# Kernel optimization log

Hardware: AMD Instinct MI355X
Metric: run time of the kernel (lower is better)

Reference implementation:

```python
import jax, jax.numpy as jnp
from jax import lax
import numpy as np

STEPSZ = 0.1
ALPHA = 0.01
BETA = 0.01
FLTRSTD = 2.0
NSTEPS = 20
DMAX = 15.0
EXTGRADFAC = 10.0
CHUNK = 32  # node chunk size for distance-map render


def _gauss_edge_fltr(std):
    # Gaussian-derivative edge filters, one per spatial axis: [2, 1, K, K]
    r = int(np.ceil(3 * std))
    x = np.arange(-r, r + 1, dtype=np.float32)
    g = np.exp(-x ** 2 / (2 * std ** 2)).astype(np.float32)
    g /= g.sum()
    dg = (-x / std ** 2) * g
    f0 = np.outer(dg, g)   # d/d(axis0)
    f1 = np.outer(g, dg)   # d/d(axis1)
    return np.stack([f0, f1])[:, None].astype(np.float32)


def _snake_matrix(n, alpha, beta, stepsz):
    # implicit internal-energy step matrix (I + t*(alpha*D2 + beta*D2@D2))^-1, open chain
    D = 2 * np.eye(n) - np.eye(n, k=1) - np.eye(n, k=-1)
    D[0, 0] = 1.0
    D[-1, -1] = 1.0
    A = alpha * D + beta * (D @ D)
    return np.linalg.inv(np.eye(n) + stepsz * A).astype(np.float32)


def _bilerp(img, pts):
    # img [H,W], pts [N,2] (row, col) -> [N]
    H, W = img.shape
    r = jnp.clip(pts[:, 0], 0.0, H - 1.0)
    c = jnp.clip(pts[:, 1], 0.0, W - 1.0)
    r0 = jnp.floor(r).astype(jnp.int32)
    c0 = jnp.floor(c).astype(jnp.int32)
    r1 = jnp.minimum(r0 + 1, H - 1)
    c1 = jnp.minimum(c0 + 1, W - 1)
    fr = r - r0
    fc = c - c0
    return (img[r0, c0] * (1 - fr) * (1 - fc) + img[r1, c0] * fr * (1 - fc)
            + img[r0, c1] * (1 - fr) * fc + img[r1, c1] * fr * fc)


def setup_inputs() -> dict:
    key = jax.random.key(0)
    k1, k2, k3 = jax.random.split(key, 3)
    B, H, W, N = 8, 512, 512, 256
    pred_dmap = jax.random.normal(k1, (B, 1, H, W), dtype=jnp.float32)
    node_pos = jax.random.uniform(k2, (B, N, 2), dtype=jnp.float32) * jnp.array([H - 1.0, W - 1.0], dtype=jnp.float32)
    widths = jax.random.uniform(k3, (B, N), dtype=jnp.float32) * 3.0 + 1.0
    return {"pred_dmap": pred_dmap, "node_pos": node_pos, "widths": widths}


def reference(pred_dmap, node_pos, widths):
    B, _, H, W = pred_dmap.shape
    N = node_pos.shape[1]

    # gradient image: conv with Gaussian-derivative filters, scaled (cmptGradIm)
    fltr = jnp.asarray(_gauss_edge_fltr(FLTRSTD))
    gimg = lax.conv_general_dilated(
        pred_dmap, fltr, (1, 1), 'SAME',
        dimension_numbers=('NCHW', 'OIHW', 'NCHW')) * EXTGRADFAC  # [B,2,H,W]

    M = jnp.asarray(_snake_matrix(N, ALPHA, BETA, STEPSZ))  # [N,N]

    def force(g, pts):  # g [2,H,W], pts [N,2] -> [N,2]
        return jnp.stack([_bilerp(g[0], pts), _bilerp(g[1], pts)], axis=-1)

    force_b = jax.vmap(force)
    bounds = jnp.array([H - 1.0, W - 1.0], dtype=pred_dmap.dtype)

    def opt_step(pos, _):
        f = force_b(gimg, pos)                                   # [B,N,2]
        pos = jnp.einsum('nm,bmd->bnd', M, pos + STEPSZ * f)
        pos = jnp.clip(pos, 0.0, bounds)
        return pos, None

    pos, _ = lax.scan(opt_step, node_pos, None, length=NSTEPS)

    ys = jnp.arange(H, dtype=pred_dmap.dtype)
    xs = jnp.arange(W, dtype=pred_dmap.dtype)

    def render(p, w):  # p [N,2], w [N] -> [H,W]
        pc = p.reshape(N // CHUNK, CHUNK, 2)
        wc = w.reshape(N // CHUNK, CHUNK)

        def rstep(carry, pw):
            pp, ww = pw  # [C,2], [C]
            d = jnp.sqrt((ys[None, :, None] - pp[:, 0, None, None]) ** 2
                         + (xs[None, None, :] - pp[:, 1, None, None]) ** 2) - ww[:, None, None]
            return jnp.minimum(carry, d.min(0)), None

        dm, _ = lax.scan(rstep, jnp.full((H, W), DMAX, dtype=p.dtype), (pc, wc))
        return jnp.clip(dm, 0.0, DMAX)

    snake_dm = jax.vmap(render)(pos, widths)[:, None]  # [B,1,H,W]
    snake_dm = lax.stop_gradient(snake_dm)             # torch.no_grad in original
    return jnp.mean((pred_dmap - snake_dm) ** 2)
```

## Files before the change

kernel.cpp:

```cpp
#include <hip/hip_runtime.h>
#include <math.h>

#define HH 512
#define WW 512
#define NB 8
#define NN 256
#define KR 6
#define KS 13

struct MBand { float c[NN][17]; };

constexpr double Dd_c(int i, int j) {
    if (i < 0 || i >= NN || j < 0 || j >= NN) return 0.0;
    if (i == j) return (i == 0 || i == NN - 1) ? 1.0 : 2.0;
    int d = i - j;
    if (d == 1 || d == -1) return -1.0;
    return 0.0;
}

constexpr MBand make_mband() {
    MBand mb{};
    double xb[NN][5] = {};
    for (int n = 0; n < NN; ++n)
        for (int d = 0; d < 5; ++d) {
            int j = n + d - 2;
            double d2 = 0.0;
            for (int k = n - 1; k <= n + 1; ++k) d2 += Dd_c(n, k) * Dd_c(k, j);
            xb[n][d] = 0.1 * (0.01 * Dd_c(n, j) + 0.01 * d2);
        }
    for (int n = 0; n < NN; ++n) {
        double acc[17] = {};
        double cur[17] = {};
        acc[8] = 1.0; cur[8] = 1.0;
        double sign = -1.0;
        for (int k = 1; k <= 4; ++k) {
            double nxt[17] = {};
            int lo = -2 * k, hi = 2 * k;
            for (int tp = lo; tp <= hi; ++tp) {
                int j = n + tp;
                double s = 0.0;
                if (j >= 0 && j < NN) {
                    for (int t = tp - 2; t <= tp + 2; ++t) {
                        if (t < -8 || t > 8) continue;
                        int m = n + t;
                        if (m < 0 || m >= NN) continue;
                        s += cur[8 + t] * xb[m][(tp - t) + 2];
                    }
                }
                nxt[8 + tp] = s;
            }
            for (int q = 0; q < 17; ++q) { cur[q] = nxt[q]; acc[q] += sign * nxt[q]; }
            sign = -sign;
        }
        for (int q = 0; q < 17; ++q) mb.c[n][q] = (float)acc[q];
    }
    return mb;
}

__device__ __constant__ MBand d_mband = make_mband();

__global__ __launch_bounds__(256) void conv_kernel(const float* __restrict__ pred,
                                                   float2* __restrict__ gimg2,
                                                   float* __restrict__ out) {
    __shared__ float tin[44][44];
    __shared__ float midG[44][32];
    __shared__ float midD[44][32];

    const int b    = blockIdx.x & 7;
    const int tile = blockIdx.x >> 3;
    const int ty0  = (tile >> 4) * 32;
    const int tx0  = (tile & 15) * 32;
    const int t    = threadIdx.x;

    if (blockIdx.x == 0 && t == 0) out[0] = 0.f;

    float g[KS], dg[KS];
    float s = 0.f;
#pragma unroll
    for (int i = 0; i < KS; ++i) {
        float x = (float)(i - KR);
        g[i] = expf(-x * x / 8.f);
        s += g[i];
    }
#pragma unroll
    for (int i = 0; i < KS; ++i) {
        g[i] /= s;
        dg[i] = (-(float)(i - KR) / 4.f) * g[i];
    }

    const float* img = pred + (size_t)b * HH * WW;

    for (int idx = t; idx < 44 * 44; idx += 256) {
        int ly = idx / 44, lx = idx % 44;
        int gy = ty0 + ly - KR, gx = tx0 + lx - KR;
        float v = 0.f;
        if (gy >= 0 && gy < HH && gx >= 0 && gx < WW) v = img[gy * WW + gx];
        tin[ly][lx] = v;
    }
    __syncthreads();

    for (int idx = t; idx < 44 * 32; idx += 256) {
        int ly = idx / 32, ox = idx % 32;
        float aG = 0.f, aD = 0.f;
#pragma unroll
        for (int k = 0; k < KS; ++k) {
            float v = tin[ly][ox + k];
            aG += v * g[k];
            aD += v * dg[k];
        }
        midG[ly][ox] = aG;
        midD[ly][ox] = aD;
    }
    __syncthreads();

    float2* outp = gimg2 + (size_t)b * HH * WW;
    for (int idx = t; idx < 32 * 32; idx += 256) {
        int oy = idx / 32, ox = idx % 32;
        float a0 = 0.f, a1 = 0.f;
#pragma unroll
        for (int k = 0; k < KS; ++k) {
            a0 += midG[oy + k][ox] * dg[k];
            a1 += midD[oy + k][ox] * g[k];
        }
        int gy = ty0 + oy, gx = tx0 + ox;
        outp[gy * WW + gx] = make_float2(10.f * a0, 10.f * a1);
    }
}

__global__ __launch_bounds__(64, 1) void snake_kernel(const float2* __restrict__ gimg2,
                                                      const float* __restrict__ node_pos,
                                                      float* __restrict__ pos_out) {
    const int batch = blockIdx.x & 7;
    const int chunk = blockIdx.x >> 3;
    const int l = threadIdx.x;
    const int nidx = chunk * 32 - 8 + l;
    const int cidx = min(max(nidx, 0), NN - 1);

    const float2* gp = gimg2 + (size_t)batch * HH * WW;

    float2 pp = ((const float2*)node_pos)[batch * NN + cidx];
    float p0 = pp.x, p1 = pp.y;

    float mbc[17];
#pragma unroll
    for (int t = 0; t < 17; ++t) mbc[t] = d_mband.c[cidx][t];

    for (int step = 0; step < 20; ++step) {
        float r = fminf(fmaxf(p0, 0.f), (float)(HH - 1));
        float c = fminf(fmaxf(p1, 0.f), (float)(WW - 1));
        float rf = floorf(r), cf = floorf(c);
        int r0 = (int)rf, c0 = (int)cf;
        int r1 = min(r0 + 1, HH - 1), c1 = min(c0 + 1, WW - 1);
        float fr = r - rf, fc = c - cf;
        float2 v00 = gp[r0 * WW + c0];
        float2 v01 = gp[r0 * WW + c1];
        float2 v10 = gp[r1 * WW + c0];
        float2 v11 = gp[r1 * WW + c1];
        float w00 = (1.f - fr) * (1.f - fc), w01 = (1.f - fr) * fc;
        float w10 = fr * (1.f - fc),         w11 = fr * fc;
        float q0 = p0 + 0.1f * (w00 * v00.x + w01 * v01.x + w10 * v10.x + w11 * v11.x);
        float q1 = p1 + 0.1f * (w00 * v00.y + w01 * v01.y + w10 * v10.y + w11 * v11.y);

        float a0 = mbc[8] * q0;
        float a1 = mbc[8] * q1;
#pragma unroll
        for (int d = 1; d <= 8; ++d) {
            float u0 = __shfl_up(q0, d),   u1 = __shfl_up(q1, d);
            float w0 = __shfl_down(q0, d), w1 = __shfl_down(q1, d);
            a0 += mbc[8 - d] * u0 + mbc[8 + d] * w0;
            a1 += mbc[8 - d] * u1 + mbc[8 + d] * w1;
        }
        p0 = fminf(fmaxf(a0, 0.f), (float)(HH - 1));
        p1 = fminf(fmaxf(a1, 0.f), (float)(WW - 1));
    }

    if (l >= 8 && l < 40)
        ((float2*)pos_out)[batch * NN + nidx] = make_float2(p0, p1);
}

__global__ __launch_bounds__(256) void render_loss_kernel(const float* __restrict__ pred,
                                                          const float* __restrict__ pos,
                                                          const float* __restrict__ widths,
                                                          float* __restrict__ out) {
    __shared__ float sl0[NN], sl1[NN], slw[NN];
    __shared__ int cnt;
    __shared__ float wred[4];

    const int b    = blockIdx.x & 7;
    const int tile = blockIdx.x >> 3;
    const int ty0  = (tile >> 4) * 32;
    const int tx0  = (tile & 15) * 32;
    const int t    = threadIdx.x;

    if (t == 0) cnt = 0;
    __syncthreads();

    {
        float p0 = pos[(b * NN + t) * 2 + 0];
        float p1 = pos[(b * NN + t) * 2 + 1];
        float w  = widths[b * NN + t];
        float dy = fmaxf(fmaxf((float)ty0 - p0, p0 - (float)(ty0 + 31)), 0.f);
        float dx = fmaxf(fmaxf((float)tx0 - p1, p1 - (float)(tx0 + 31)), 0.f);
        float rr = 15.f + w;
        if (dy * dy + dx * dx <= rr * rr) {
            int i = atomicAdd(&cnt, 1);
            sl0[i] = p0; sl1[i] = p1; slw[i] = w;
        }
    }
    __syncthreads();
    const int c = cnt;

    const int oy = t >> 3;
    const int ox = (t & 7) * 4;
    const float fy = (float)(ty0 + oy);
    const float fx = (float)(tx0 + ox);

    float dm0 = 15.f, dm1 = 15.f, dm2 = 15.f, dm3 = 15.f;
    for (int j = 0; j < c; ++j) {
        float dy  = fy - sl0[j];
        float dy2 = dy * dy;
        float w   = slw[j];
        float dx  = fx - sl1[j];
        dm0 = fminf(dm0, __builtin_amdgcn_sqrtf(dy2 + dx * dx) - w);
        dx += 1.f;
        dm1 = fminf(dm1, __builtin_amdgcn_sqrtf(dy2 + dx * dx) - w);
        dx += 1.f;
        dm2 = fminf(dm2, __builtin_amdgcn_sqrtf(dy2 + dx * dx) - w);
        dx += 1.f;
        dm3 = fminf(dm3, __builtin_amdgcn_sqrtf(dy2 + dx * dx) - w);
    }
    dm0 = fminf(fmaxf(dm0, 0.f), 15.f);
    dm1 = fminf(fmaxf(dm1, 0.f), 15.f);
    dm2 = fminf(fmaxf(dm2, 0.f), 15.f);
    dm3 = fminf(fmaxf(dm3, 0.f), 15.f);

    const float4 pv = *(const float4*)(pred + (size_t)b * HH * WW
                                       + (ty0 + oy) * WW + (tx0 + ox));
    float e0 = pv.x - dm0, e1 = pv.y - dm1, e2 = pv.z - dm2, e3 = pv.w - dm3;
    float acc = (e0 * e0 + e1 * e1 + e2 * e2 + e3 * e3)
              * (1.0f / (float)(NB * HH * WW));

#pragma unroll
    for (int m = 1; m < 64; m <<= 1) acc += __shfl_xor(acc, m);
    if ((t & 63) == 0) wred[t >> 6] = acc;
    __syncthreads();
    if (t == 0) atomicAdd(out, wred[0] + wred[1] + wred[2] + wred[3]);
}

extern "C" void kernel_launch(void* const* d_in, const int* in_sizes, int n_in,
                              void* d_out, int out_size, void* d_ws, size_t ws_size,
                              hipStream_t stream) {
    const float* pred     = (const float*)d_in[0];
    const float* node_pos = (const float*)d_in[1];
    const float* widths   = (const float*)d_in[2];
    float* out = (float*)d_out;

    float2* gimg2  = (float2*)d_ws;
    float* pos_out = (float*)d_ws + (size_t)NB * 2 * HH * WW;

    conv_kernel<<<NB * 256, 256, 0, stream>>>(pred, gimg2, out);

    snake_kernel<<<NB * 8, 64, 0, stream>>>(gimg2, node_pos, pos_out);

    render_loss_kernel<<<NB * 256, 256, 0, stream>>>(pred, pos_out, widths, out);
}
```

Measured before the change: 54.37 us.

## Fuse conv and snake kernels using per-batch atomic completion counters

Merges the gradient convolution and the snake optimisation into one launch. The first 64 blocks, after doing their conv tile, spin-wait on a per-batch global atomic counter until all 256 conv tiles of that batch are finished, then run the snake iterations. The aim is to remove one kernel launch boundary and let the snake work overlap with the tail of the conv. It relies on all conv blocks of a batch eventually being scheduled while the waiting blocks spin, and it uses device-global counters that are reset by the last finishing block.

```diff
diff --git a/kernel.cpp b/kernel.cpp
--- a/kernel.cpp
+++ b/kernel.cpp
@@ -59,9 +59,14 @@
 
 __device__ __constant__ MBand d_mband = make_mband();
 
-__global__ __launch_bounds__(256) void conv_kernel(const float* __restrict__ pred,
-                                                   float2* __restrict__ gimg2,
-                                                   float* __restrict__ out) {
+__device__ unsigned g_cnt[NB]  = {};
+__device__ unsigned g_done[NB] = {};
+
+__global__ __launch_bounds__(256) void conv_snake_kernel(const float* __restrict__ pred,
+                                                         const float* __restrict__ node_pos,
+                                                         float2* __restrict__ gimg2,
+                                                         float* __restrict__ pos_out,
+                                                         float* __restrict__ out) {
     __shared__ float tin[44][44];
     __shared__ float midG[44][32];
     __shared__ float midD[44][32];
@@ -74,108 +79,134 @@
 
     if (blockIdx.x == 0 && t == 0) out[0] = 0.f;
 
-    float g[KS], dg[KS];
-    float s = 0.f;
-#pragma unroll
-    for (int i = 0; i < KS; ++i) {
-        float x = (float)(i - KR);
-        g[i] = expf(-x * x / 8.f);
-        s += g[i];
-    }
-#pragma unroll
-    for (int i = 0; i < KS; ++i) {
-        g[i] /= s;
-        dg[i] = (-(float)(i - KR) / 4.f) * g[i];
-    }
-
-    const float* img = pred + (size_t)b * HH * WW;
-
-    for (int idx = t; idx < 44 * 44; idx += 256) {
-        int ly = idx / 44, lx = idx % 44;
-        int gy = ty0 + ly - KR, gx = tx0 + lx - KR;
-        float v = 0.f;
-        if (gy >= 0 && gy < HH && gx >= 0 && gx < WW) v = img[gy * WW + gx];
-        tin[ly][lx] = v;
-    }
-    __syncthreads();
-
-    for (int idx = t; idx < 44 * 32; idx += 256) {
-        int ly = idx / 32, ox = idx % 32;
-        float aG = 0.f, aD = 0.f;
-#pragma unroll
-        for (int k = 0; k < KS; ++k) {
-            float v = tin[ly][ox + k];
-            aG += v * g[k];
-            aD += v * dg[k];
-        }
-        midG[ly][ox] = aG;
-        midD[ly][ox] = aD;
-    }
-    __syncthreads();
-
-    float2* outp = gimg2 + (size_t)b * HH * WW;
-    for (int idx = t; idx < 32 * 32; idx += 256) {
-        int oy = idx / 32, ox = idx % 32;
-        float a0 = 0.f, a1 = 0.f;
-#pragma unroll
-        for (int k = 0; k < KS; ++k) {
-            a0 += midG[oy + k][ox] * dg[k];
-            a1 += midD[oy + k][ox] * g[k];
-        }
-        int gy = ty0 + oy, gx = tx0 + ox;
-        outp[gy * WW + gx] = make_float2(10.f * a0, 10.f * a1);
-    }
-}
-
-__global__ __launch_bounds__(64, 1) void snake_kernel(const float2* __restrict__ gimg2,
-                                                      const float* __restrict__ node_pos,
-                                                      float* __restrict__ pos_out) {
-    const int batch = blockIdx.x & 7;
-    const int chunk = blockIdx.x >> 3;
-    const int l = threadIdx.x;
-    const int nidx = chunk * 32 - 8 + l;
-    const int cidx = min(max(nidx, 0), NN - 1);
-
-    const float2* gp = gimg2 + (size_t)batch * HH * WW;
-
-    float2 pp = ((const float2*)node_pos)[batch * NN + cidx];
-    float p0 = pp.x, p1 = pp.y;
-
-    float mbc[17];
-#pragma unroll
-    for (int t = 0; t < 17; ++t) mbc[t] = d_mband.c[cidx][t];
-
-    for (int step = 0; step < 20; ++step) {
-        float r = fminf(fmaxf(p0, 0.f), (float)(HH - 1));
-        float c = fminf(fmaxf(p1, 0.f), (float)(WW - 1));
-        float rf = floorf(r), cf = floorf(c);
-        int r0 = (int)rf, c0 = (int)cf;
-        int r1 = min(r0 + 1, HH - 1), c1 = min(c0 + 1, WW - 1);
-        float fr = r - rf, fc = c - cf;
-        float2 v00 = gp[r0 * WW + c0];
-        float2 v01 = gp[r0 * WW + c1];
-        float2 v10 = gp[r1 * WW + c0];
-        float2 v11 = gp[r1 * WW + c1];
-        float w00 = (1.f - fr) * (1.f - fc), w01 = (1.f - fr) * fc;
-        float w10 = fr * (1.f - fc),         w11 = fr * fc;
-        float q0 = p0 + 0.1f * (w00 * v00.x + w01 * v01.x + w10 * v10.x + w11 * v11.x);
-        float q1 = p1 + 0.1f * (w00 * v00.y + w01 * v01.y + w10 * v10.y + w11 * v11.y);
-
-        float a0 = mbc[8] * q0;
-        float a1 = mbc[8] * q1;
-#pragma unroll
-        for (int d = 1; d <= 8; ++d) {
-            float u0 = __shfl_up(q0, d),   u1 = __shfl_up(q1, d);
-            float w0 = __shfl_down(q0, d), w1 = __shfl_down(q1, d);
-            a0 += mbc[8 - d] * u0 + mbc[8 + d] * w0;
-            a1 += mbc[8 - d] * u1 + mbc[8 + d] * w1;
-        }
-        p0 = fminf(fmaxf(a0, 0.f), (float)(HH - 1));
-        p1 = fminf(fmaxf(a1, 0.f), (float)(WW - 1));
-    }
-
-    if (l >= 8 && l < 40)
-        ((float2*)pos_out)[batch * NN + nidx] = make_float2(p0, p1);
+    {
+        float g[KS], dg[KS];
+        float s = 0.f;
+#pragma unroll
+        for (int i = 0; i < KS; ++i) {
+            float x = (float)(i - KR);
+            g[i] = expf(-x * x / 8.f);
+            s += g[i];
+        }
+#pragma unroll
+        for (int i = 0; i < KS; ++i) {
+            g[i] /= s;
+            dg[i] = (-(float)(i - KR) / 4.f) * g[i];
+        }
+
+        const float* img = pred + (size_t)b * HH * WW;
+
+        for (int idx = t; idx < 44 * 44; idx += 256) {
+            int ly = idx / 44, lx = idx % 44;
+            int gy = ty0 + ly - KR, gx = tx0 + lx - KR;
+            float v = 0.f;
+            if (gy >= 0 && gy < HH && gx >= 0 && gx < WW) v = img[gy * WW + gx];
+            tin[ly][lx] = v;
+        }
+        __syncthreads();
+
+        for (int idx = t; idx < 44 * 32; idx += 256) {
+            int ly = idx / 32, ox = idx % 32;
+            float aG = 0.f, aD = 0.f;
+#pragma unroll
+            for (int k = 0; k < KS; ++k) {
+                float v = tin[ly][ox + k];
+                aG += v * g[k];
+                aD += v * dg[k];
+            }
+            midG[ly][ox] = aG;
+            midD[ly][ox] = aD;
+        }
+        __syncthreads();
+
+        float2* outp = gimg2 + (size_t)b * HH * WW;
+        for (int idx = t; idx < 32 * 32; idx += 256) {
+            int oy = idx / 32, ox = idx % 32;
+            float a0 = 0.f, a1 = 0.f;
+#pragma unroll
+            for (int k = 0; k < KS; ++k) {
+                a0 += midG[oy + k][ox] * dg[k];
+                a1 += midD[oy + k][ox] * g[k];
+            }
+            outp[(ty0 + oy) * WW + (tx0 + ox)] = make_float2(10.f * a0, 10.f * a1);
+        }
+    }
+
+    __syncthreads();
+    if (t == 0)
+        __hip_atomic_fetch_add(&g_cnt[b], 1u, __ATOMIC_RELEASE,
+                               __HIP_MEMORY_SCOPE_AGENT);
+
+    if (blockIdx.x >= 64) return;
+
+    if (t == 0) {
+        while (__hip_atomic_load(&g_cnt[b], __ATOMIC_RELAXED,
+                                 __HIP_MEMORY_SCOPE_AGENT) < 256u)
+            __builtin_amdgcn_s_sleep(8);
+        (void)__hip_atomic_load(&g_cnt[b], __ATOMIC_ACQUIRE,
+                                __HIP_MEMORY_SCOPE_AGENT);
+    }
+    __syncthreads();
+
+    if (t < 64) {
+        const int chunk = tile;
+        const int l = t;
+        const int nidx = chunk * 32 - 8 + l;
+        const int cidx = min(max(nidx, 0), NN - 1);
+
+        const float2* gp = gimg2 + (size_t)b * HH * WW;
+
+        float2 pp = ((const float2*)node_pos)[b * NN + cidx];
+        float p0 = pp.x, p1 = pp.y;
+
+        float mbc[17];
+#pragma unroll
+        for (int k = 0; k < 17; ++k) mbc[k] = d_mband.c[cidx][k];
+
+        for (int step = 0; step < 20; ++step) {
+            float r = fminf(fmaxf(p0, 0.f), (float)(HH - 1));
+            float c = fminf(fmaxf(p1, 0.f), (float)(WW - 1));
+            float rf = floorf(r), cf = floorf(c);
+            int r0 = (int)rf, c0 = (int)cf;
+            int r1 = min(r0 + 1, HH - 1), c1 = min(c0 + 1, WW - 1);
+            float fr = r - rf, fc = c - cf;
+            float2 v00 = gp[r0 * WW + c0];
+            float2 v01 = gp[r0 * WW + c1];
+            float2 v10 = gp[r1 * WW + c0];
+            float2 v11 = gp[r1 * WW + c1];
+            float w00 = (1.f - fr) * (1.f - fc), w01 = (1.f - fr) * fc;
+            float w10 = fr * (1.f - fc),         w11 = fr * fc;
+            float q0 = p0 + 0.1f * (w00 * v00.x + w01 * v01.x + w10 * v10.x + w11 * v11.x);
+            float q1 = p1 + 0.1f * (w00 * v00.y + w01 * v01.y + w10 * v10.y + w11 * v11.y);
+
+            float a0 = mbc[8] * q0;
+            float a1 = mbc[8] * q1;
+#pragma unroll
+            for (int d = 1; d <= 8; ++d) {
+                float u0 = __shfl_up(q0, d),   u1 = __shfl_up(q1, d);
+                float w0 = __shfl_down(q0, d), w1 = __shfl_down(q1, d);
+                a0 += mbc[8 - d] * u0 + mbc[8 + d] * w0;
+                a1 += mbc[8 - d] * u1 + mbc[8 + d] * w1;
+            }
+            p0 = fminf(fmaxf(a0, 0.f), (float)(HH - 1));
+            p1 = fminf(fmaxf(a1, 0.f), (float)(WW - 1));
+        }
+
+        if (l >= 8 && l < 40)
+            ((float2*)pos_out)[b * NN + nidx] = make_float2(p0, p1);
+    }
+
+    __syncthreads();
+    if (t == 0) {
+        unsigned d = __hip_atomic_fetch_add(&g_done[b], 1u, __ATOMIC_ACQ_REL,
+                                            __HIP_MEMORY_SCOPE_AGENT);
+        if (d == 7u) {
+            __hip_atomic_store(&g_cnt[b], 0u, __ATOMIC_RELAXED,
+                               __HIP_MEMORY_SCOPE_AGENT);
+            __hip_atomic_store(&g_done[b], 0u, __ATOMIC_RELAXED,
+                               __HIP_MEMORY_SCOPE_AGENT);
+        }
+    }
 }
 
 __global__ __launch_bounds__(256) void render_loss_kernel(const float* __restrict__ pred,
@@ -258,9 +289,8 @@
     float2* gimg2  = (float2*)d_ws;
     float* pos_out = (float*)d_ws + (size_t)NB * 2 * HH * WW;
 
-    conv_kernel<<<NB * 256, 256, 0, stream>>>(pred, gimg2, out);
-
-    snake_kernel<<<NB * 8, 64, 0, stream>>>(gimg2, node_pos, pos_out);
+    conv_snake_kernel<<<NB * 256, 256, 0, stream>>>(pred, node_pos,
+                                                    gimg2, pos_out, out);
 
     render_loss_kernel<<<NB * 256, 256, 0, stream>>>(pred, pos_out, widths, out);
 }
```

After: 108.7 us. 100.0% more time.
